# Kernel tuning notes

Measured on AMD Instinct MI355X. Metric: run time of the kernel, lower is better.

## Reference

```python
import jax, jax.numpy as jnp
import numpy as np
import jax.scipy.special as jsp

N_RESERVOIR = 8192
N_INPUT = 64
N_LAYERS = 3
INPUT_SCALE = 0.4
RES_SCALE = 0.9
BIAS_SCALE = 0.1
ALPHA = 1.0  # activation_fn_args = (1.0,)
N_HADAMARD = 1 << int(np.ceil(np.log2(N_INPUT + N_RESERVOIR)))  # 16384
N_PADDING = N_HADAMARD - N_RESERVOIR - N_INPUT
BATCH = 512


def fwht(x):
    """Fast Walsh-Hadamard transform along last axis. x: [B, n], n a power of 2."""
    B, n = x.shape
    h = 1
    while h < n:
        x = x.reshape(B, n // (2 * h), 2, h)
        a = x[:, :, 0, :]
        b = x[:, :, 1, :]
        x = jnp.concatenate([a + b, a - b], axis=-1).reshape(B, n)
        h *= 2
    return x


def leaky_erf(x, state, alpha):
    return (1.0 - alpha) * state + alpha * jsp.erf(x)


def setup_inputs() -> dict:
    key = jax.random.key(0)
    k1, k2, k3, k4 = jax.random.split(key, 4)
    state = jax.random.normal(k1, (BATCH, N_RESERVOIR), dtype=jnp.float32)
    inputs = jax.random.normal(k2, (BATCH, N_INPUT), dtype=jnp.float32)
    bias = BIAS_SCALE * jax.random.normal(k3, (N_RESERVOIR,), dtype=jnp.float32)
    # structured-transform diagonals: random Rademacher signs, one per layer
    diag = jnp.where(jax.random.uniform(k4, (N_LAYERS, N_HADAMARD)) < 0.5, -1.0, 1.0).astype(jnp.float32)
    return {"state": state, "inputs": inputs, "bias": bias, "diag": diag}


def reference(state, inputs, bias, diag):
    B = state.shape[0]
    pad = jnp.zeros((B, N_PADDING), dtype=state.dtype)
    X = jnp.concatenate([RES_SCALE * state, INPUT_SCALE * inputs, pad], axis=1)  # [B, N_HADAMARD]
    for l in range(N_LAYERS):
        X = fwht(X * diag[l])
    z = X[:, :N_RESERVOIR] / N_HADAMARD + bias
    return leaky_erf(z, state, ALPHA)
```

## Files before the change

### kernel.cpp

```cpp
#include <hip/hip_runtime.h>
#include <math.h>

#define NH    16384
#define NRES  8192
#define NINP  64
#define BATCH 512

typedef float v2f __attribute__((ext_vector_type(2)));

__device__ __forceinline__ constexpr int gfold(int v) {
    return ((v >> 5) & 7) ^ ((v >> 8) & 7) ^ ((v >> 11) & 7);
}
__device__ __forceinline__ constexpr int physf(int v) {
    return v ^ (gfold(v) << 2);
}

__device__ __forceinline__ v2f pk_add(v2f a, v2f b) {
    v2f d;
    asm("v_pk_add_f32 %0, %1, %2" : "=v"(d) : "v"(a), "v"(b));
    return d;
}
__device__ __forceinline__ v2f pk_sub(v2f a, v2f b, v2f negone) {
    v2f d;
    asm("v_pk_fma_f32 %0, %1, %2, %3" : "=v"(d) : "v"(b), "v"(negone), "v"(a));
    return d;
}

template <int T>
__device__ __forceinline__ void pstage(v2f X[32], v2f negone) {
#pragma unroll
    for (int p = 0; p < 32; ++p) {
        if (!(p & T)) {
            v2f A = X[p], B = X[p | T];
            X[p]     = pk_add(A, B);
            X[p | T] = pk_sub(A, B, negone);
        }
    }
}
__device__ __forceinline__ void vstage0(v2f X[32]) {
#pragma unroll
    for (int p = 0; p < 32; ++p) {
        float a = X[p].x, b = X[p].y;
        X[p].x = a + b;
        X[p].y = a - b;
    }
}

template <int CTRL>
__device__ __forceinline__ float dppf(float v) {
    return __builtin_bit_cast(float,
        __builtin_amdgcn_update_dpp(0, __builtin_bit_cast(int, v), CTRL, 0xF, 0xF, true));
}
template <int CTRL>
__device__ __forceinline__ void dpp_swap(float A, float B, bool odd, float& oA, float& oB) {
    float dA = dppf<CTRL>(A), dB = dppf<CTRL>(B);
    oA = odd ? dB : A;
    oB = odd ? B  : dA;
}
__device__ __forceinline__ void pl16_swap(float& a, float& b) {
    asm("v_permlane16_swap_b32 %0, %1" : "+v"(a), "+v"(b));
}
__device__ __forceinline__ void pl32_swap(float& a, float& b) {
    asm("v_permlane32_swap_b32 %0, %1" : "+v"(a), "+v"(b));
}

__device__ __forceinline__ void shuffle_exchange(v2f X[32], bool odd0, bool odd1) {
#pragma unroll
    for (int p = 0; p < 32; ++p) if (!(p & 2)) {
        float a0, a1, b0, b1;
        dpp_swap<0xB1>(X[p].x, X[p | 2].x, odd0, a0, b0);
        dpp_swap<0xB1>(X[p].y, X[p | 2].y, odd0, a1, b1);
        X[p] = (v2f){a0, a1}; X[p | 2] = (v2f){b0, b1};
    }
#pragma unroll
    for (int p = 0; p < 32; ++p) if (!(p & 4)) {
        float a0, a1, b0, b1;
        dpp_swap<0x4E>(X[p].x, X[p | 4].x, odd1, a0, b0);
        dpp_swap<0x4E>(X[p].y, X[p | 4].y, odd1, a1, b1);
        X[p] = (v2f){a0, a1}; X[p | 4] = (v2f){b0, b1};
    }
#pragma unroll
    for (int p = 0; p < 32; ++p) if (!(p & 8)) {
        float a = X[p].x, b = X[p | 8].x; pl16_swap(a, b); X[p].x = a; X[p | 8].x = b;
        float c = X[p].y, d = X[p | 8].y; pl16_swap(c, d); X[p].y = c; X[p | 8].y = d;
    }
#pragma unroll
    for (int p = 0; p < 32; ++p) if (!(p & 16)) {
        float a = X[p].x, b = X[p | 16].x; pl32_swap(a, b); X[p].x = a; X[p | 16].x = b;
        float c = X[p].y, d = X[p | 16].y; pl32_swap(c, d); X[p].y = c; X[p | 16].y = d;
    }
}

#define WRX(Q, SH) do { _Pragma("unroll") \
    for (int j = 0; j < 16; ++j) \
        lds4[(unsigned)((Q) ^ physf(j << (SH))) >> 2] = \
            make_float4(X[2*j].x, X[2*j].y, X[2*j+1].x, X[2*j+1].y); } while (0)

#define RDX(Q, SH) do { _Pragma("unroll") \
    for (int j = 0; j < 16; ++j) { \
        float4 v = lds4[(unsigned)((Q) ^ physf(j << (SH))) >> 2]; \
        X[2*j]   = (v2f){v.x, v.y}; \
        X[2*j+1] = (v2f){v.z, v.w}; } } while (0)

#define DIAG_APPLY(PF) do { _Pragma("unroll") \
    for (int j = 0; j < 16; ++j) { \
        X[2*j]   *= (v2f){(PF)[j].x, (PF)[j].y}; \
        X[2*j+1] *= (v2f){(PF)[j].z, (PF)[j].w}; \
    } } while (0)

#define BAR() asm volatile("s_waitcnt lgkmcnt(0)\n\ts_barrier" ::: "memory")

__device__ __forceinline__ float erf_fast(float z) {
    float p = z * z;
    float u = z * fmaf(p, 0.10090f, 1.1283793f);
    float e = __builtin_amdgcn_exp2f(u * 2.8853902f);
    float r = __builtin_amdgcn_rcpf(e + 1.0f);
    return fmaf(-2.0f, r, 1.0f);
}


__global__ __launch_bounds__(256, 2) void st_kernel(
    const float* __restrict__ state, const float* __restrict__ inputs,
    const float* __restrict__ bias,  const float* __restrict__ diag,
    float* __restrict__ out)
{
    __shared__ float4 lds4[NH / 4];
    const int t = threadIdx.x;
    const int r = blockIdx.x;
    const int l = t & 63, w = t >> 6;
    const int l01 = l & 3, l23 = (l >> 2) & 3, l45 = (l >> 4) & 3;
    const bool odd0 = (l & 1), odd1 = (l & 2);

    const int bA = (w << 12) | (l23 << 10) | (l45 << 8) | (l01 << 6);
    const int bB = (w << 12) | (l23 << 10) | (l45 << 4) | (l01 << 2);
    const int bC = (w << 8)  | (l23 << 6)  | (l45 << 4) | (l01 << 2);
    const int bD = (l45 << 12) | (l01 << 10) | (w << 8) | (l23 << 6);

    const v2f negone = (v2f){-1.0f, -1.0f};

    v2f X[32];

    if (t < 128) {
        const float* srow = state + (size_t)r * NRES + bA;
        const float* d0   = diag + bA;
#pragma unroll
        for (int h = 0; h < 2; ++h) {
            float4 sv[8], dv[8];
#pragma unroll
            for (int k = 0; k < 8; ++k) {
                sv[k] = *(const float4*)(srow + 4 * (h * 8 + k));
                dv[k] = *(const float4*)(d0   + 4 * (h * 8 + k));
            }
#pragma unroll
            for (int k = 0; k < 8; ++k) {
                const int j = h * 8 + k;
                X[2*j]   = (v2f){0.9f * sv[k].x * dv[k].x, 0.9f * sv[k].y * dv[k].y};
                X[2*j+1] = (v2f){0.9f * sv[k].z * dv[k].z, 0.9f * sv[k].w * dv[k].w};
            }
        }
    } else if (t == 128) {
        const float* irow = inputs + r * NINP;
        const float* d0   = diag + NRES;
#pragma unroll
        for (int j = 0; j < 16; ++j) {
            float4 v = *(const float4*)(irow + 4 * j);
            float4 d = *(const float4*)(d0 + 4 * j);
            X[2*j]   = (v2f){0.4f * v.x * d.x, 0.4f * v.y * d.y};
            X[2*j+1] = (v2f){0.4f * v.z * d.z, 0.4f * v.w * d.w};
        }
    } else {
#pragma unroll
        for (int p = 0; p < 32; ++p) X[p] = (v2f){0.f, 0.f};
    }

    vstage0(X); pstage<1>(X, negone); pstage<2>(X, negone);
    pstage<4>(X, negone); pstage<8>(X, negone); pstage<16>(X, negone);

    float4 pf1[16];
    {
        const float* d1 = diag + NH + bC;
#pragma unroll
        for (int j = 0; j < 16; ++j) pf1[j] = *(const float4*)(d1 + (j << 10));
    }

    shuffle_exchange(X, odd0, odd1);
    pstage<2>(X, negone); pstage<4>(X, negone);
    pstage<8>(X, negone); pstage<16>(X, negone);

    { const int Q = physf(bB); WRX(Q, 6); }
    BAR();
    { const int Q = physf(bC); RDX(Q, 10); }
    pstage<2>(X, negone); pstage<4>(X, negone);
    pstage<8>(X, negone); pstage<16>(X, negone);
    DIAG_APPLY(pf1);
    vstage0(X); pstage<1>(X, negone);
    pstage<2>(X, negone); pstage<4>(X, negone);
    pstage<8>(X, negone); pstage<16>(X, negone);

    float4 pf2[16];
    {
        const float* d2 = diag + 2 * NH + bB;
#pragma unroll
        for (int j = 0; j < 16; ++j) pf2[j] = *(const float4*)(d2 + (j << 6));
    }

    shuffle_exchange(X, odd0, odd1);
    pstage<2>(X, negone); pstage<4>(X, negone);
    pstage<8>(X, negone); pstage<16>(X, negone);

    BAR();
    { const int Q = physf(bD); WRX(Q, 2); }
    BAR();
    { const int Q = physf(bB); RDX(Q, 6); }
    pstage<2>(X, negone); pstage<4>(X, negone);
    pstage<8>(X, negone); pstage<16>(X, negone);
    DIAG_APPLY(pf2);
    vstage0(X); pstage<1>(X, negone);
    pstage<2>(X, negone); pstage<4>(X, negone);
    pstage<8>(X, negone); pstage<16>(X, negone);

    float4 bv[8];
#pragma unroll
    for (int j = 0; j < 8; ++j) bv[j] = *(const float4*)(bias + bC + (j << 10));

    shuffle_exchange(X, odd0, odd1);
    pstage<2>(X, negone); pstage<4>(X, negone);
    pstage<8>(X, negone); pstage<16>(X, negone);

    BAR();
    { const int Q = physf(bA); WRX(Q, 2); }
    BAR();
    { const int Q = physf(bC); RDX(Q, 10); }
    pstage<2>(X, negone); pstage<4>(X, negone);
    pstage<8>(X, negone); pstage<16>(X, negone);

    {
        float* orow = out + (size_t)r * NRES;
        const float inv = 1.0f / (float)NH;
#pragma unroll
        for (int j = 0; j < 8; ++j) {
            float4 o;
            o.x = erf_fast(fmaf(X[2*j].x,   inv, bv[j].x));
            o.y = erf_fast(fmaf(X[2*j].y,   inv, bv[j].y));
            o.z = erf_fast(fmaf(X[2*j+1].x, inv, bv[j].z));
            o.w = erf_fast(fmaf(X[2*j+1].y, inv, bv[j].w));
            *(float4*)(orow + bC + (j << 10)) = o;
        }
    }
}

extern "C" void kernel_launch(void* const* d_in, const int* in_sizes, int n_in,
                              void* d_out, int out_size, void* d_ws, size_t ws_size,
                              hipStream_t stream) {
    (void)in_sizes; (void)n_in; (void)out_size; (void)d_ws; (void)ws_size;
    const float* state  = (const float*)d_in[0];
    const float* inputs = (const float*)d_in[1];
    const float* bias   = (const float*)d_in[2];
    const float* diag   = (const float*)d_in[3];
    float* out = (float*)d_out;

    hipLaunchKernelGGL(st_kernel, dim3(BATCH), dim3(256), 0, stream,
                       state, inputs, bias, diag, out);
}
```

Measured before the change: 25.45 us.

## Split each row's FWHT across 512 threads with 32 elements per thread

```diff
diff --git a/kernel.cpp b/kernel.cpp
--- a/kernel.cpp
+++ b/kernel.cpp
@@ -27,9 +27,9 @@
 }
 
 template <int T>
-__device__ __forceinline__ void pstage(v2f X[32], v2f negone) {
-#pragma unroll
-    for (int p = 0; p < 32; ++p) {
+__device__ __forceinline__ void pstage(v2f X[16], v2f negone) {
+#pragma unroll
+    for (int p = 0; p < 16; ++p) {
         if (!(p & T)) {
             v2f A = X[p], B = X[p | T];
             X[p]     = pk_add(A, B);
@@ -37,13 +37,16 @@
         }
     }
 }
-__device__ __forceinline__ void vstage0(v2f X[32]) {
-#pragma unroll
-    for (int p = 0; p < 32; ++p) {
+__device__ __forceinline__ void vstage0(v2f X[16]) {
+#pragma unroll
+    for (int p = 0; p < 16; ++p) {
         float a = X[p].x, b = X[p].y;
         X[p].x = a + b;
         X[p].y = a - b;
     }
+}
+__device__ __forceinline__ void jpass(v2f X[16], v2f negone) {
+    pstage<2>(X, negone); pstage<4>(X, negone); pstage<8>(X, negone);
 }
 
 template <int CTRL>
@@ -64,48 +67,50 @@
     asm("v_permlane32_swap_b32 %0, %1" : "+v"(a), "+v"(b));
 }
 
-__device__ __forceinline__ void shuffle_exchange(v2f X[32], bool odd0, bool odd1) {
-#pragma unroll
-    for (int p = 0; p < 32; ++p) if (!(p & 2)) {
+__device__ __forceinline__ void shuffle_exchange(v2f X[16], bool odd0) {
+#pragma unroll
+    for (int p = 0; p < 16; ++p) if (!(p & 2)) {
         float a0, a1, b0, b1;
         dpp_swap<0xB1>(X[p].x, X[p | 2].x, odd0, a0, b0);
         dpp_swap<0xB1>(X[p].y, X[p | 2].y, odd0, a1, b1);
         X[p] = (v2f){a0, a1}; X[p | 2] = (v2f){b0, b1};
     }
 #pragma unroll
-    for (int p = 0; p < 32; ++p) if (!(p & 4)) {
-        float a0, a1, b0, b1;
-        dpp_swap<0x4E>(X[p].x, X[p | 4].x, odd1, a0, b0);
-        dpp_swap<0x4E>(X[p].y, X[p | 4].y, odd1, a1, b1);
-        X[p] = (v2f){a0, a1}; X[p | 4] = (v2f){b0, b1};
-    }
-#pragma unroll
-    for (int p = 0; p < 32; ++p) if (!(p & 8)) {
-        float a = X[p].x, b = X[p | 8].x; pl16_swap(a, b); X[p].x = a; X[p | 8].x = b;
-        float c = X[p].y, d = X[p | 8].y; pl16_swap(c, d); X[p].y = c; X[p | 8].y = d;
-    }
-#pragma unroll
-    for (int p = 0; p < 32; ++p) if (!(p & 16)) {
-        float a = X[p].x, b = X[p | 16].x; pl32_swap(a, b); X[p].x = a; X[p | 16].x = b;
-        float c = X[p].y, d = X[p | 16].y; pl32_swap(c, d); X[p].y = c; X[p | 16].y = d;
-    }
-}
-
-#define WRX(Q, SH) do { _Pragma("unroll") \
-    for (int j = 0; j < 16; ++j) \
-        lds4[(unsigned)((Q) ^ physf(j << (SH))) >> 2] = \
-            make_float4(X[2*j].x, X[2*j].y, X[2*j+1].x, X[2*j+1].y); } while (0)
-
-#define RDX(Q, SH) do { _Pragma("unroll") \
-    for (int j = 0; j < 16; ++j) { \
-        float4 v = lds4[(unsigned)((Q) ^ physf(j << (SH))) >> 2]; \
-        X[2*j]   = (v2f){v.x, v.y}; \
-        X[2*j+1] = (v2f){v.z, v.w}; } } while (0)
-
-#define DIAG_APPLY(PF) do { _Pragma("unroll") \
-    for (int j = 0; j < 16; ++j) { \
-        X[2*j]   *= (v2f){(PF)[j].x, (PF)[j].y}; \
-        X[2*j+1] *= (v2f){(PF)[j].z, (PF)[j].w}; \
+    for (int p = 0; p < 16; ++p) if (!(p & 4)) {
+        float a = X[p].x, b = X[p | 4].x; pl16_swap(a, b); X[p].x = a; X[p | 4].x = b;
+        float c = X[p].y, d = X[p | 4].y; pl16_swap(c, d); X[p].y = c; X[p | 4].y = d;
+    }
+#pragma unroll
+    for (int p = 0; p < 16; ++p) if (!(p & 8)) {
+        float a = X[p].x, b = X[p | 8].x; pl32_swap(a, b); X[p].x = a; X[p | 8].x = b;
+        float c = X[p].y, d = X[p | 8].y; pl32_swap(c, d); X[p].y = c; X[p | 8].y = d;
+    }
+}
+
+#define GOFF(g, G0, G1, G2) \
+    (((g) & 1 ? (G0) : 0) | ((g) & 2 ? (G1) : 0) | ((g) & 4 ? (G2) : 0))
+
+#define WRX(Q, G0, G1, G2) do { _Pragma("unroll") \
+    for (int g = 0; g < 8; ++g) \
+        lds4[(unsigned)((Q) ^ physf(GOFF(g, G0, G1, G2))) >> 2] = \
+            make_float4(X[2*g].x, X[2*g].y, X[2*g+1].x, X[2*g+1].y); } while (0)
+
+#define RDX(Q, G0, G1, G2) do { _Pragma("unroll") \
+    for (int g = 0; g < 8; ++g) { \
+        float4 v = lds4[(unsigned)((Q) ^ physf(GOFF(g, G0, G1, G2))) >> 2]; \
+        X[2*g]   = (v2f){v.x, v.y}; \
+        X[2*g+1] = (v2f){v.z, v.w}; } } while (0)
+
+#define DIAG_MUL(BASE, G0, G1, G2) do { _Pragma("unroll") \
+    for (int h = 0; h < 2; ++h) { \
+        float4 dv[4]; \
+        _Pragma("unroll") for (int k = 0; k < 4; ++k) \
+            dv[k] = *(const float4*)((BASE) + GOFF(h * 4 + k, G0, G1, G2)); \
+        _Pragma("unroll") for (int k = 0; k < 4; ++k) { \
+            const int g = h * 4 + k; \
+            X[2*g]   *= (v2f){dv[k].x, dv[k].y}; \
+            X[2*g+1] *= (v2f){dv[k].z, dv[k].w}; \
+        } \
     } } while (0)
 
 #define BAR() asm volatile("s_waitcnt lgkmcnt(0)\n\ts_barrier" ::: "memory")
@@ -118,8 +123,7 @@
     return fmaf(-2.0f, r, 1.0f);
 }
 
-
-__global__ __launch_bounds__(256, 2) void st_kernel(
+__global__ __launch_bounds__(512, 2) void st_kernel(
     const float* __restrict__ state, const float* __restrict__ inputs,
     const float* __restrict__ bias,  const float* __restrict__ diag,
     float* __restrict__ out)
@@ -128,123 +132,107 @@
     const int t = threadIdx.x;
     const int r = blockIdx.x;
     const int l = t & 63, w = t >> 6;
-    const int l01 = l & 3, l23 = (l >> 2) & 3, l45 = (l >> 4) & 3;
-    const bool odd0 = (l & 1), odd1 = (l & 2);
-
-    const int bA = (w << 12) | (l23 << 10) | (l45 << 8) | (l01 << 6);
-    const int bB = (w << 12) | (l23 << 10) | (l45 << 4) | (l01 << 2);
-    const int bC = (w << 8)  | (l23 << 6)  | (l45 << 4) | (l01 << 2);
-    const int bD = (l45 << 12) | (l01 << 10) | (w << 8) | (l23 << 6);
+    const int l0 = l & 1, l1 = (l >> 1) & 1, l2 = (l >> 2) & 1;
+    const int l3 = (l >> 3) & 1, l4 = (l >> 4) & 1, l5 = (l >> 5) & 1;
+    const int w0 = w & 1, w1 = (w >> 1) & 1, w2 = (w >> 2) & 1;
+    const bool odd0 = l0;
+
+    const int b_w1 = l0*4 + l4*8 + l5*16 + l1*64 + l2*128 + l3*256
+                   + w0*2048 + w1*4096 + w2*8192;
+    const int b_r1 = w0*4 + w1*8 + w2*16 + l1*32 + l0*64 + l4*128
+                   + l5*256 + l2*512 + l3*1024;
+    const int b_r2 = l0*32 + w0*64 + w1*128 + w2*256 + l4*512
+                   + l5*1024 + l1*2048 + l2*4096 + l3*8192;
+    const int b_r3 = l1*4 + l2*8 + l3*16 + w0*32 + w1*512 + w2*1024
+                   + l0*2048 + l4*4096 + l5*8192;
+    const int b_d1 = w0*4 + w1*8 + w2*16 + l1*32 + l2*512 + l3*1024
+                   + l0*2048 + l4*4096 + l5*8192;
+    const int b_d2 = l0*4 + l4*8 + l5*16 + w0*64 + w1*128 + w2*256
+                   + l1*2048 + l2*4096 + l3*8192;
+    const int b_st = l1*4 + l2*8 + l3*16 + w0*32 + l0*64 + l4*128
+                   + l5*256 + w1*512 + w2*1024;
 
     const v2f negone = (v2f){-1.0f, -1.0f};
-
-    v2f X[32];
-
-    if (t < 128) {
-        const float* srow = state + (size_t)r * NRES + bA;
-        const float* d0   = diag + bA;
-#pragma unroll
-        for (int h = 0; h < 2; ++h) {
-            float4 sv[8], dv[8];
-#pragma unroll
-            for (int k = 0; k < 8; ++k) {
-                sv[k] = *(const float4*)(srow + 4 * (h * 8 + k));
-                dv[k] = *(const float4*)(d0   + 4 * (h * 8 + k));
-            }
-#pragma unroll
-            for (int k = 0; k < 8; ++k) {
-                const int j = h * 8 + k;
-                X[2*j]   = (v2f){0.9f * sv[k].x * dv[k].x, 0.9f * sv[k].y * dv[k].y};
-                X[2*j+1] = (v2f){0.9f * sv[k].z * dv[k].z, 0.9f * sv[k].w * dv[k].w};
-            }
-        }
-    } else if (t == 128) {
-        const float* irow = inputs + r * NINP;
-        const float* d0   = diag + NRES;
-#pragma unroll
-        for (int j = 0; j < 16; ++j) {
-            float4 v = *(const float4*)(irow + 4 * j);
-            float4 d = *(const float4*)(d0 + 4 * j);
-            X[2*j]   = (v2f){0.4f * v.x * d.x, 0.4f * v.y * d.y};
-            X[2*j+1] = (v2f){0.4f * v.z * d.z, 0.4f * v.w * d.w};
+    v2f X[16];
+
+    if (t < 256) {
+        const float* srow = state + (size_t)r * NRES + t * 32;
+        const float* d0   = diag + t * 32;
+#pragma unroll
+        for (int g = 0; g < 8; ++g) {
+            float4 v = *(const float4*)(srow + 4 * g);
+            float4 d = *(const float4*)(d0 + 4 * g);
+            X[2*g]   = (v2f){0.9f * v.x * d.x, 0.9f * v.y * d.y};
+            X[2*g+1] = (v2f){0.9f * v.z * d.z, 0.9f * v.w * d.w};
+        }
+    } else if (t < 258) {
+        const float* irow = inputs + r * NINP + (t - 256) * 32;
+        const float* d0   = diag + t * 32;
+#pragma unroll
+        for (int g = 0; g < 8; ++g) {
+            float4 v = *(const float4*)(irow + 4 * g);
+            float4 d = *(const float4*)(d0 + 4 * g);
+            X[2*g]   = (v2f){0.4f * v.x * d.x, 0.4f * v.y * d.y};
+            X[2*g+1] = (v2f){0.4f * v.z * d.z, 0.4f * v.w * d.w};
         }
     } else {
 #pragma unroll
-        for (int p = 0; p < 32; ++p) X[p] = (v2f){0.f, 0.f};
-    }
-
-    vstage0(X); pstage<1>(X, negone); pstage<2>(X, negone);
-    pstage<4>(X, negone); pstage<8>(X, negone); pstage<16>(X, negone);
-
-    float4 pf1[16];
-    {
-        const float* d1 = diag + NH + bC;
-#pragma unroll
-        for (int j = 0; j < 16; ++j) pf1[j] = *(const float4*)(d1 + (j << 10));
-    }
-
-    shuffle_exchange(X, odd0, odd1);
-    pstage<2>(X, negone); pstage<4>(X, negone);
-    pstage<8>(X, negone); pstage<16>(X, negone);
-
-    { const int Q = physf(bB); WRX(Q, 6); }
-    BAR();
-    { const int Q = physf(bC); RDX(Q, 10); }
-    pstage<2>(X, negone); pstage<4>(X, negone);
-    pstage<8>(X, negone); pstage<16>(X, negone);
-    DIAG_APPLY(pf1);
+        for (int p = 0; p < 16; ++p) X[p] = (v2f){0.f, 0.f};
+    }
+
     vstage0(X); pstage<1>(X, negone);
-    pstage<2>(X, negone); pstage<4>(X, negone);
-    pstage<8>(X, negone); pstage<16>(X, negone);
-
-    float4 pf2[16];
-    {
-        const float* d2 = diag + 2 * NH + bB;
-#pragma unroll
-        for (int j = 0; j < 16; ++j) pf2[j] = *(const float4*)(d2 + (j << 6));
-    }
-
-    shuffle_exchange(X, odd0, odd1);
-    pstage<2>(X, negone); pstage<4>(X, negone);
-    pstage<8>(X, negone); pstage<16>(X, negone);
-
-    BAR();
-    { const int Q = physf(bD); WRX(Q, 2); }
-    BAR();
-    { const int Q = physf(bB); RDX(Q, 6); }
-    pstage<2>(X, negone); pstage<4>(X, negone);
-    pstage<8>(X, negone); pstage<16>(X, negone);
-    DIAG_APPLY(pf2);
+    jpass(X, negone);
+    shuffle_exchange(X, odd0);
+    jpass(X, negone);
+
+    { const int Q = physf(b_w1); WRX(Q, 32, 512, 1024); }
+    BAR();
+    { const int Q = physf(b_r1); RDX(Q, 2048, 4096, 8192); }
+    jpass(X, negone);
+    shuffle_exchange(X, odd0);
+    jpass(X, negone);
+
+    DIAG_MUL(diag + NH + b_d1, 64, 128, 256);
     vstage0(X); pstage<1>(X, negone);
-    pstage<2>(X, negone); pstage<4>(X, negone);
-    pstage<8>(X, negone); pstage<16>(X, negone);
-
-    float4 bv[8];
-#pragma unroll
-    for (int j = 0; j < 8; ++j) bv[j] = *(const float4*)(bias + bC + (j << 10));
-
-    shuffle_exchange(X, odd0, odd1);
-    pstage<2>(X, negone); pstage<4>(X, negone);
-    pstage<8>(X, negone); pstage<16>(X, negone);
-
-    BAR();
-    { const int Q = physf(bA); WRX(Q, 2); }
-    BAR();
-    { const int Q = physf(bC); RDX(Q, 10); }
-    pstage<2>(X, negone); pstage<4>(X, negone);
-    pstage<8>(X, negone); pstage<16>(X, negone);
+    jpass(X, negone);
+    shuffle_exchange(X, odd0);
+    jpass(X, negone);
+
+    BAR();
+    { const int Q = physf(b_r1); WRX(Q, 2048, 4096, 8192); }
+    BAR();
+    { const int Q = physf(b_r2); RDX(Q, 4, 8, 16); }
+    jpass(X, negone);
+    shuffle_exchange(X, odd0);
+    jpass(X, negone);
+
+    DIAG_MUL(diag + 2 * NH + b_d2, 32, 512, 1024);
+    vstage0(X); pstage<1>(X, negone);
+    jpass(X, negone);
+    shuffle_exchange(X, odd0);
+    jpass(X, negone);
+
+    BAR();
+    { const int Q = physf(b_r2); WRX(Q, 4, 8, 16); }
+    BAR();
+    { const int Q = physf(b_r3); RDX(Q, 64, 128, 256); }
+    jpass(X, negone);
+    shuffle_exchange(X, odd0);
+    jpass(X, negone);
 
     {
         float* orow = out + (size_t)r * NRES;
         const float inv = 1.0f / (float)NH;
 #pragma unroll
-        for (int j = 0; j < 8; ++j) {
+        for (int g = 0; g < 4; ++g) {
+            const int a = b_st + (g & 1) * 2048 + (g >> 1) * 4096;
+            float4 b = *(const float4*)(bias + a);
             float4 o;
-            o.x = erf_fast(fmaf(X[2*j].x,   inv, bv[j].x));
-            o.y = erf_fast(fmaf(X[2*j].y,   inv, bv[j].y));
-            o.z = erf_fast(fmaf(X[2*j+1].x, inv, bv[j].z));
-            o.w = erf_fast(fmaf(X[2*j+1].y, inv, bv[j].w));
-            *(float4*)(orow + bC + (j << 10)) = o;
+            o.x = erf_fast(fmaf(X[2*g].x,   inv, b.x));
+            o.y = erf_fast(fmaf(X[2*g].y,   inv, b.y));
+            o.z = erf_fast(fmaf(X[2*g+1].x, inv, b.z));
+            o.w = erf_fast(fmaf(X[2*g+1].y, inv, b.w));
+            *(float4*)(orow + a) = o;
         }
     }
 }
@@ -259,6 +247,6 @@
     const float* diag   = (const float*)d_in[3];
     float* out = (float*)d_out;
 
-    hipLaunchKernelGGL(st_kernel, dim3(BATCH), dim3(256), 0, stream,
+    hipLaunchKernelGGL(st_kernel, dim3(BATCH), dim3(512), 0, stream,
                        state, inputs, bias, diag, out);
 }
```

New measurement: 27.07 us. +6.4%, slower.
